# Performance work log

Hardware: AMD Instinct MI355X
Metric: run time of the kernel (lower is better)

Reference implementation:

```python
import jax, jax.numpy as jnp
import numpy as np

NX, NY = 1024, 512
LX, LY = 0.26, 0.12
NU = 1e-4
U_INLET = 0.1
DX = LX / (NX - 1)
DY = LY / (NY - 1)
W_CONT, W_MOM, W_BC = 1.0, 0.1, 1.0


def _pad_x(f):
    # replicate pad along x axis (dim -2)
    return jnp.pad(f, ((0, 0), (0, 0), (1, 1), (0, 0)), mode='edge')


def _pad_y(f):
    return jnp.pad(f, ((0, 0), (0, 0), (0, 0), (1, 1)), mode='edge')


def ddx(f):
    p = _pad_x(f)
    return (p[:, :, 2:, :] - p[:, :, :-2, :]) / (2.0 * DX)


def ddy(f):
    p = _pad_y(f)
    return (p[:, :, :, 2:] - p[:, :, :, :-2]) / (2.0 * DY)


def d2dx2(f):
    p = _pad_x(f)
    return (p[:, :, 2:, :] - 2.0 * f + p[:, :, :-2, :]) / (DX * DX)


def d2dy2(f):
    p = _pad_y(f)
    return (p[:, :, :, 2:] - 2.0 * f + p[:, :, :, :-2]) / (DY * DY)


def masked_mean(x, mask):
    return (x * mask).sum() / jnp.maximum(mask.sum(), 1.0)


def region_masks(x_in):
    r = x_in[:, 1:2].astype(jnp.float32)  # [B,1,NX,NY] region codes
    fluid = (r > 0.5).astype(jnp.float32)
    obstacle = (r < 0.5).astype(jnp.float32)
    wall = ((r > 1.5) & (r < 2.5)).astype(jnp.float32)
    inlet = ((r > 2.5) & (r < 3.5)).astype(jnp.float32)
    outlet = (r > 3.5).astype(jnp.float32)
    noslip = ((obstacle + wall) > 0.5).astype(jnp.float32)
    # interior = fluid with zeroed 1-cell border
    border = jnp.zeros((NX, NY), jnp.float32).at[1:-1, 1:-1].set(1.0)
    interior = fluid * border
    return fluid, interior, noslip, inlet, outlet


def setup_inputs() -> dict:
    key = jax.random.key(0)
    k1, k2 = jax.random.split(key)
    y_hat = jax.random.normal(k1, (16, 3, NX, NY), dtype=jnp.float32)
    x_in = jax.random.randint(k2, (16, 2, NX, NY), 0, 5).astype(jnp.int32)
    return {'y_hat': y_hat, 'x_in': x_in}


def reference(y_hat, x_in):
    ux = y_hat[:, 0:1]
    uy = y_hat[:, 1:2]
    p = y_hat[:, 2:3]
    fluid, interior, noslip, inlet, outlet = region_masks(x_in)

    # continuity
    div = ddx(ux) + ddy(uy)
    l_cont = masked_mean(div ** 2, interior)

    # momentum
    res_x = ux * ddx(ux) + uy * ddy(ux) + ddx(p) - NU * (d2dx2(ux) + d2dy2(ux))
    res_y = ux * ddx(uy) + uy * ddy(uy) + ddy(p) - NU * (d2dx2(uy) + d2dy2(uy))
    l_mom = masked_mean(res_x ** 2, interior) + masked_mean(res_y ** 2, interior)

    # boundary (masked_mean already returns 0 for empty masks via denom clamp)
    l_bc = masked_mean(ux ** 2, noslip) + masked_mean(uy ** 2, noslip)
    l_bc = l_bc + masked_mean((ux - U_INLET) ** 2, inlet) + masked_mean(uy ** 2, inlet)
    l_bc = l_bc + masked_mean(ddx(ux) ** 2, outlet)

    total = W_CONT * l_cont + W_MOM * l_mom + W_BC * l_bc
    return jnp.stack([l_cont, l_mom, l_bc, total])
```

## Files before the change

### kernel.cpp

```cpp
#include <hip/hip_runtime.h>


namespace {
constexpr int NXc   = 1024;
constexpr int NYc   = 512;
constexpr int NXYc  = NXc * NYc;
constexpr int NBc   = 16;
constexpr int NTHR  = 256;
constexpr int NACC  = 10;
constexpr int RROWS = 8;
constexpr int NCHUNK = NXc / RROWS;
constexpr int NWAVE  = NBc * NCHUNK;
constexpr int NBLK   = NWAVE / (NTHR / 64);
}

struct Frow { float4 xl, xh, yl, yh, pl, ph; };

__device__ __forceinline__ Frow ldrow(const float* __restrict__ ux,
                                      const float* __restrict__ uy,
                                      const float* __restrict__ pp, int off) {
  Frow f;
  f.xl = *reinterpret_cast<const float4*>(ux + off);
  f.xh = *reinterpret_cast<const float4*>(ux + off + 4);
  f.yl = *reinterpret_cast<const float4*>(uy + off);
  f.yh = *reinterpret_cast<const float4*>(uy + off + 4);
  f.pl = *reinterpret_cast<const float4*>(pp + off);
  f.ph = *reinterpret_cast<const float4*>(pp + off + 4);
  return f;
}

__global__ __launch_bounds__(NTHR, 2) void pil_main(const float* __restrict__ y,
                                                    const int* __restrict__ xin,
                                                    double* __restrict__ partial) {
  constexpr double DXd = 0.26 / 1023.0;
  constexpr double DYd = 0.12 / 511.0;
  const float INV2DX = (float)(1.0 / (2.0 * DXd));
  const float INV2DY = (float)(1.0 / (2.0 * DYd));
  const float INVDX2 = (float)(1.0 / (DXd * DXd));
  const float INVDY2 = (float)(1.0 / (DYd * DYd));
  constexpr float NU = 1e-4f;
  constexpr float U_INLET = 0.1f;

  const int l     = threadIdx.x & 63;
  const int wv    = (blockIdx.x << 2) | (threadIdx.x >> 6);
  const int chunk = wv & (NCHUNK - 1);
  const int b     = wv >> 7;
  const int i0    = chunk * RROWS;
  const int jc    = l << 3;

  const float* __restrict__ ux = y + (size_t)b * 3 * NXYc;
  const float* __restrict__ uy = ux + NXYc;
  const float* __restrict__ pp = ux + 2 * NXYc;
  const int*   __restrict__ rp = xin + (size_t)(2 * b + 1) * NXYc;

  float a[NACC];
#pragma unroll
  for (int k = 0; k < NACC; ++k) a[k] = 0.f;

  Frow P = ldrow(ux, uy, pp, (i0 > 0 ? i0 - 1 : 0) * NYc + jc);
  Frow C = ldrow(ux, uy, pp, i0 * NYc + jc);
  Frow N = ldrow(ux, uy, pp, (i0 + 1) * NYc + jc);
  int4 rCl = *reinterpret_cast<const int4*>(rp + i0 * NYc + jc);
  int4 rCh = *reinterpret_cast<const int4*>(rp + i0 * NYc + jc + 4);
  int4 rNl = *reinterpret_cast<const int4*>(rp + (i0 + 1) * NYc + jc);
  int4 rNh = *reinterpret_cast<const int4*>(rp + (i0 + 1) * NYc + jc + 4);

#pragma unroll
  for (int s = 0; s < RROWS; ++s) {
    const int i = i0 + s;

    Frow F = C;
    int4 rFl = rCl, rFh = rCh;
    if (s < RROWS - 1) F = ldrow(ux, uy, pp, min(i + 2, NXc - 1) * NYc + jc);
    if (s < RROWS - 2) {
      rFl = *reinterpret_cast<const int4*>(rp + (i + 2) * NYc + jc);
      rFh = *reinterpret_cast<const int4*>(rp + (i + 2) * NYc + jc + 4);
    }

    const float cx[8] = {C.xl.x, C.xl.y, C.xl.z, C.xl.w, C.xh.x, C.xh.y, C.xh.z, C.xh.w};
    const float cy_[8] = {C.yl.x, C.yl.y, C.yl.z, C.yl.w, C.yh.x, C.yh.y, C.yh.z, C.yh.w};
    const float cp_[8] = {C.pl.x, C.pl.y, C.pl.z, C.pl.w, C.ph.x, C.ph.y, C.ph.z, C.ph.w};
    const float pxA[8] = {P.xl.x, P.xl.y, P.xl.z, P.xl.w, P.xh.x, P.xh.y, P.xh.z, P.xh.w};
    const float pyA[8] = {P.yl.x, P.yl.y, P.yl.z, P.yl.w, P.yh.x, P.yh.y, P.yh.z, P.yh.w};
    const float ppA[8] = {P.pl.x, P.pl.y, P.pl.z, P.pl.w, P.ph.x, P.ph.y, P.ph.z, P.ph.w};
    const float nxA[8] = {N.xl.x, N.xl.y, N.xl.z, N.xl.w, N.xh.x, N.xh.y, N.xh.z, N.xh.w};
    const float nyA[8] = {N.yl.x, N.yl.y, N.yl.z, N.yl.w, N.yh.x, N.yh.y, N.yh.z, N.yh.w};
    const float npA[8] = {N.pl.x, N.pl.y, N.pl.z, N.pl.w, N.ph.x, N.ph.y, N.ph.z, N.ph.w};
    const int   rA[8]  = {rCl.x, rCl.y, rCl.z, rCl.w, rCh.x, rCh.y, rCh.z, rCh.w};

    float lxx = __shfl_up(cx[7], 1, 64);   if (l == 0)  lxx = cx[0];
    float rxx = __shfl_down(cx[0], 1, 64); if (l == 63) rxx = cx[7];
    float lyy = __shfl_up(cy_[7], 1, 64);  if (l == 0)  lyy = cy_[0];
    float ryy = __shfl_down(cy_[0], 1, 64);if (l == 63) ryy = cy_[7];
    float lpp = __shfl_up(cp_[7], 1, 64);  if (l == 0)  lpp = cp_[0];
    float rpp = __shfl_down(cp_[0], 1, 64);if (l == 63) rpp = cp_[7];

    const bool irow = (i >= 1) & (i <= NXc - 2);

#pragma unroll
    for (int e = 0; e < 8; ++e) {
      const int   r    = rA[e];
      const float c_ux = cx[e], c_uy = cy_[e];
      const float uxm = (e == 0) ? lxx : cx[e - 1];
      const float uxp = (e == 7) ? rxx : cx[e + 1];
      const float uym = (e == 0) ? lyy : cy_[e - 1];
      const float uyp = (e == 7) ? ryy : cy_[e + 1];
      const float pm_ = (e == 0) ? lpp : cp_[e - 1];
      const float pp_ = (e == 7) ? rpp : cp_[e + 1];

      const float ddx_ux = (nxA[e] - pxA[e]) * INV2DX;
      const float ddy_ux = (uxp - uxm) * INV2DY;
      const float ddx_uy = (nyA[e] - pyA[e]) * INV2DX;
      const float ddy_uy = (uyp - uym) * INV2DY;

      const bool jedge = ((l == 0) & (e == 0)) | ((l == 63) & (e == 7));
      const bool interior = (r >= 1) & irow & (!jedge);
      if (interior) {
        const float dv    = ddx_ux + ddy_uy;
        const float d2xux = (nxA[e] - 2.f * c_ux + pxA[e]) * INVDX2;
        const float d2yux = (uxp - 2.f * c_ux + uxm) * INVDY2;
        const float d2xuy = (nyA[e] - 2.f * c_uy + pyA[e]) * INVDX2;
        const float d2yuy = (uyp - 2.f * c_uy + uym) * INVDY2;
        const float ddx_p = (npA[e] - ppA[e]) * INV2DX;
        const float ddy_p = (pp_ - pm_) * INV2DY;
        const float rx = c_ux * ddx_ux + c_uy * ddy_ux + ddx_p - NU * (d2xux + d2yux);
        const float ry = c_ux * ddx_uy + c_uy * ddy_uy + ddy_p - NU * (d2xuy + d2yuy);
        a[0] += dv * dv;
        a[1] += rx * rx;
        a[2] += ry * ry;
        a[3] += 1.f;
      }
      if ((r == 0) | (r == 2)) {
        a[4] += c_ux * c_ux + c_uy * c_uy;
        a[5] += 1.f;
      }
      if (r == 3) {
        const float d = c_ux - U_INLET;
        a[6] += d * d + c_uy * c_uy;
        a[7] += 1.f;
      }
      if (r == 4) {
        a[8] += ddx_ux * ddx_ux;
        a[9] += 1.f;
      }
    }

    if (s < RROWS - 1) {
      P = C; C = N; N = F;
      rCl = rNl; rCh = rNh; rNl = rFl; rNh = rFh;
    }
  }

#pragma unroll
  for (int k = 0; k < NACC; ++k) {
    float v = a[k];
#pragma unroll
    for (int off = 32; off > 0; off >>= 1) v += __shfl_down(v, off, 64);
    a[k] = v;
  }

  __shared__ double sacc[NTHR / 64][NACC];
  const int lane = threadIdx.x & 63;
  const int wave = threadIdx.x >> 6;
  if (lane == 0) {
#pragma unroll
    for (int k = 0; k < NACC; ++k) sacc[wave][k] = (double)a[k];
  }
  __syncthreads();
  if (threadIdx.x < NACC) {
    double s = 0.0;
#pragma unroll
    for (int w = 0; w < NTHR / 64; ++w) s += sacc[w][threadIdx.x];
    partial[threadIdx.x * gridDim.x + blockIdx.x] = s;
  }
}

__global__ __launch_bounds__(NTHR) void pil_finalize(const double* __restrict__ partial,
                                                     float* __restrict__ out, int nblk) {
  __shared__ double sw[NACC][NTHR / 64];
  const int t = threadIdx.x;
  const int lane = t & 63, wave = t >> 6;
#pragma unroll
  for (int k = 0; k < NACC; ++k) {
    double v = 0.0;
    for (int b = t; b < nblk; b += NTHR) v += partial[k * nblk + b];
#pragma unroll
    for (int off = 32; off > 0; off >>= 1) v += __shfl_down(v, off, 64);
    if (lane == 0) sw[k][wave] = v;
  }
  __syncthreads();
  if (t == 0) {
    double acc[NACC];
#pragma unroll
    for (int k = 0; k < NACC; ++k) {
      double s = 0.0;
#pragma unroll
      for (int w = 0; w < NTHR / 64; ++w) s += sw[k][w];
      acc[k] = s;
    }
    const double l_cont = acc[0] / fmax(acc[3], 1.0);
    const double l_mom  = (acc[1] + acc[2]) / fmax(acc[3], 1.0);
    const double l_bc   = acc[4] / fmax(acc[5], 1.0)
                        + acc[6] / fmax(acc[7], 1.0)
                        + acc[8] / fmax(acc[9], 1.0);
    const double total  = 1.0 * l_cont + 0.1 * l_mom + 1.0 * l_bc;
    out[0] = (float)l_cont;
    out[1] = (float)l_mom;
    out[2] = (float)l_bc;
    out[3] = (float)total;
  }
}

extern "C" void kernel_launch(void* const* d_in, const int* in_sizes, int n_in,
                              void* d_out, int out_size, void* d_ws, size_t ws_size,
                              hipStream_t stream) {
  const float* y   = (const float*)d_in[0];
  const int*   xin = (const int*)d_in[1];
  double* partial  = (double*)d_ws;

  pil_main<<<NBLK, NTHR, 0, stream>>>(y, xin, partial);
  pil_finalize<<<1, NTHR, 0, stream>>>(partial, (float*)d_out, NBLK);
}
```

Measured before the change: 48.01 us.

## Halve rows per wave and fuse finalize via last-block ticket reduction

Cuts rows per wave from 8 to 4, doubling the grid and raising the launch-bounds occupancy hint to 4 blocks per CU. The region-code row is now loaded once per row instead of being double-buffered. The separate finalize kernel is replaced by an atomic ticket, so the last block to finish reduces all partials, with a memset added to reset the ticket each call. This aims to hide more memory latency and remove a kernel launch, at the cost of more halo-row reloads and a serial reduction over twice as many partials in one block.

New measurement: 148.4 us. +209.1%, slower.

```diff
diff --git a/kernel.cpp b/kernel.cpp
--- a/kernel.cpp
+++ b/kernel.cpp
@@ -8,7 +8,7 @@
 constexpr int NBc   = 16;
 constexpr int NTHR  = 256;
 constexpr int NACC  = 10;
-constexpr int RROWS = 8;
+constexpr int RROWS = 4;
 constexpr int NCHUNK = NXc / RROWS;
 constexpr int NWAVE  = NBc * NCHUNK;
 constexpr int NBLK   = NWAVE / (NTHR / 64);
@@ -29,9 +29,11 @@
   return f;
 }
 
-__global__ __launch_bounds__(NTHR, 2) void pil_main(const float* __restrict__ y,
+__global__ __launch_bounds__(NTHR, 4) void pil_main(const float* __restrict__ y,
                                                     const int* __restrict__ xin,
-                                                    double* __restrict__ partial) {
+                                                    double* __restrict__ partial,
+                                                    unsigned int* __restrict__ ticket,
+                                                    float* __restrict__ out) {
   constexpr double DXd = 0.26 / 1023.0;
   constexpr double DYd = 0.12 / 511.0;
   const float INV2DX = (float)(1.0 / (2.0 * DXd));
@@ -44,7 +46,7 @@
   const int l     = threadIdx.x & 63;
   const int wv    = (blockIdx.x << 2) | (threadIdx.x >> 6);
   const int chunk = wv & (NCHUNK - 1);
-  const int b     = wv >> 7;
+  const int b     = wv >> 8;
   const int i0    = chunk * RROWS;
   const int jc    = l << 3;
 
@@ -62,8 +64,6 @@
   Frow N = ldrow(ux, uy, pp, (i0 + 1) * NYc + jc);
   int4 rCl = *reinterpret_cast<const int4*>(rp + i0 * NYc + jc);
   int4 rCh = *reinterpret_cast<const int4*>(rp + i0 * NYc + jc + 4);
-  int4 rNl = *reinterpret_cast<const int4*>(rp + (i0 + 1) * NYc + jc);
-  int4 rNh = *reinterpret_cast<const int4*>(rp + (i0 + 1) * NYc + jc + 4);
 
 #pragma unroll
   for (int s = 0; s < RROWS; ++s) {
@@ -71,13 +71,13 @@
 
     Frow F = C;
     int4 rFl = rCl, rFh = rCh;
-    if (s < RROWS - 1) F = ldrow(ux, uy, pp, min(i + 2, NXc - 1) * NYc + jc);
-    if (s < RROWS - 2) {
-      rFl = *reinterpret_cast<const int4*>(rp + (i + 2) * NYc + jc);
-      rFh = *reinterpret_cast<const int4*>(rp + (i + 2) * NYc + jc + 4);
-    }
-
-    const float cx[8] = {C.xl.x, C.xl.y, C.xl.z, C.xl.w, C.xh.x, C.xh.y, C.xh.z, C.xh.w};
+    if (s < RROWS - 1) {
+      F = ldrow(ux, uy, pp, min(i + 2, NXc - 1) * NYc + jc);
+      rFl = *reinterpret_cast<const int4*>(rp + (i + 1) * NYc + jc);
+      rFh = *reinterpret_cast<const int4*>(rp + (i + 1) * NYc + jc + 4);
+    }
+
+    const float cx[8]  = {C.xl.x, C.xl.y, C.xl.z, C.xl.w, C.xh.x, C.xh.y, C.xh.z, C.xh.w};
     const float cy_[8] = {C.yl.x, C.yl.y, C.yl.z, C.yl.w, C.yh.x, C.yh.y, C.yh.z, C.yh.w};
     const float cp_[8] = {C.pl.x, C.pl.y, C.pl.z, C.pl.w, C.ph.x, C.ph.y, C.ph.z, C.ph.w};
     const float pxA[8] = {P.xl.x, P.xl.y, P.xl.z, P.xl.w, P.xh.x, P.xh.y, P.xh.z, P.xh.w};
@@ -88,12 +88,12 @@
     const float npA[8] = {N.pl.x, N.pl.y, N.pl.z, N.pl.w, N.ph.x, N.ph.y, N.ph.z, N.ph.w};
     const int   rA[8]  = {rCl.x, rCl.y, rCl.z, rCl.w, rCh.x, rCh.y, rCh.z, rCh.w};
 
-    float lxx = __shfl_up(cx[7], 1, 64);   if (l == 0)  lxx = cx[0];
-    float rxx = __shfl_down(cx[0], 1, 64); if (l == 63) rxx = cx[7];
-    float lyy = __shfl_up(cy_[7], 1, 64);  if (l == 0)  lyy = cy_[0];
-    float ryy = __shfl_down(cy_[0], 1, 64);if (l == 63) ryy = cy_[7];
-    float lpp = __shfl_up(cp_[7], 1, 64);  if (l == 0)  lpp = cp_[0];
-    float rpp = __shfl_down(cp_[0], 1, 64);if (l == 63) rpp = cp_[7];
+    float lxx = __shfl_up(cx[7], 1, 64);    if (l == 0)  lxx = cx[0];
+    float rxx = __shfl_down(cx[0], 1, 64);  if (l == 63) rxx = cx[7];
+    float lyy = __shfl_up(cy_[7], 1, 64);   if (l == 0)  lyy = cy_[0];
+    float ryy = __shfl_down(cy_[0], 1, 64); if (l == 63) ryy = cy_[7];
+    float lpp = __shfl_up(cp_[7], 1, 64);   if (l == 0)  lpp = cp_[0];
+    float rpp = __shfl_down(cp_[0], 1, 64); if (l == 63) rpp = cp_[7];
 
     const bool irow = (i >= 1) & (i <= NXc - 2);
 
@@ -106,7 +106,7 @@
       const float uym = (e == 0) ? lyy : cy_[e - 1];
       const float uyp = (e == 7) ? ryy : cy_[e + 1];
       const float pm_ = (e == 0) ? lpp : cp_[e - 1];
-      const float pp_ = (e == 7) ? rpp : cp_[e + 1];
+      const float pq_ = (e == 7) ? rpp : cp_[e + 1];
 
       const float ddx_ux = (nxA[e] - pxA[e]) * INV2DX;
       const float ddy_ux = (uxp - uxm) * INV2DY;
@@ -122,7 +122,7 @@
         const float d2xuy = (nyA[e] - 2.f * c_uy + pyA[e]) * INVDX2;
         const float d2yuy = (uyp - 2.f * c_uy + uym) * INVDY2;
         const float ddx_p = (npA[e] - ppA[e]) * INV2DX;
-        const float ddy_p = (pp_ - pm_) * INV2DY;
+        const float ddy_p = (pq_ - pm_) * INV2DY;
         const float rx = c_ux * ddx_ux + c_uy * ddy_ux + ddx_p - NU * (d2xux + d2yux);
         const float ry = c_ux * ddx_uy + c_uy * ddy_uy + ddy_p - NU * (d2xuy + d2yuy);
         a[0] += dv * dv;
@@ -147,7 +147,7 @@
 
     if (s < RROWS - 1) {
       P = C; C = N; N = F;
-      rCl = rNl; rCh = rNh; rNl = rFl; rNh = rFh;
+      rCl = rFl; rCh = rFh;
     }
   }
 
@@ -171,19 +171,23 @@
     double s = 0.0;
 #pragma unroll
     for (int w = 0; w < NTHR / 64; ++w) s += sacc[w][threadIdx.x];
-    partial[threadIdx.x * gridDim.x + blockIdx.x] = s;
-  }
-}
-
-__global__ __launch_bounds__(NTHR) void pil_finalize(const double* __restrict__ partial,
-                                                     float* __restrict__ out, int nblk) {
+    partial[threadIdx.x * NBLK + blockIdx.x] = s;
+  }
+
+  __threadfence();
+  __shared__ bool amLast;
+  if (threadIdx.x == 0)
+    amLast = (atomicAdd(ticket, 1u) == (unsigned)(NBLK - 1));
+  __syncthreads();
+  if (!amLast) return;
+  __threadfence();
+
   __shared__ double sw[NACC][NTHR / 64];
   const int t = threadIdx.x;
-  const int lane = t & 63, wave = t >> 6;
 #pragma unroll
   for (int k = 0; k < NACC; ++k) {
     double v = 0.0;
-    for (int b = t; b < nblk; b += NTHR) v += partial[k * nblk + b];
+    for (int bb = t; bb < NBLK; bb += NTHR) v += partial[k * NBLK + bb];
 #pragma unroll
     for (int off = 32; off > 0; off >>= 1) v += __shfl_down(v, off, 64);
     if (lane == 0) sw[k][wave] = v;
@@ -217,7 +221,8 @@
   const float* y   = (const float*)d_in[0];
   const int*   xin = (const int*)d_in[1];
   double* partial  = (double*)d_ws;
-
-  pil_main<<<NBLK, NTHR, 0, stream>>>(y, xin, partial);
-  pil_finalize<<<1, NTHR, 0, stream>>>(partial, (float*)d_out, NBLK);
-}
+  unsigned int* ticket = (unsigned int*)((char*)d_ws + (size_t)NACC * NBLK * 8);
+
+  hipMemsetAsync(ticket, 0, sizeof(unsigned int), stream);
+  pil_main<<<NBLK, NTHR, 0, stream>>>(y, xin, partial, ticket, (float*)d_out);
+}
```
